# Kernel tuning notes

Measured on AMD Instinct MI355X. Metric: run time of the kernel, lower is better.

## Reference

```python
import jax, jax.numpy as jnp
import numpy as np
import math

B, S, H, D = 4, 1024, 12, 64   # batch, max_seqlen, heads, head_dim
DIM = H * D                    # 768
L = 512                        # actual per-sequence length (unpadded)
NNZ = B * L                    # total non-pad tokens


def setup_inputs() -> dict:
    key = jax.random.key(0)
    k1, k2, k3 = jax.random.split(key, 3)
    hidden_states = jax.random.normal(k1, (NNZ, DIM), dtype=jnp.float32)
    Wqkv_w = jax.random.normal(k2, (3 * DIM, DIM), dtype=jnp.float32) * 0.02
    Wqkv_b = jnp.zeros((3 * DIM,), dtype=jnp.float32)
    # attn mask: first L tokens of each sequence are real
    attn_mask = (jnp.arange(S)[None, :] < L).astype(jnp.int32) * jnp.ones((B, 1), jnp.int32)
    # additive bias (e.g. ALiBi/relative-pos style) + key-padding penalty
    bias = jax.random.normal(k3, (B, H, S, S), dtype=jnp.float32) * 0.02
    bias = bias + jnp.where(attn_mask[:, None, None, :] == 1, 0.0, -10000.0)
    # flattened positions of non-pad tokens in the padded (B*S,) layout
    indices = (jnp.arange(B)[:, None] * S + jnp.arange(L)[None, :]).reshape(-1).astype(jnp.int64)
    cu_seqlens = (jnp.arange(B + 1) * L).astype(jnp.int32)
    return {
        "hidden_states": hidden_states,
        "Wqkv_w": Wqkv_w,
        "Wqkv_b": Wqkv_b,
        "bias": bias,
        "cu_seqlens": cu_seqlens,
        "max_seqlen_in_batch": S,
        "indices": indices,
        "attn_mask": attn_mask,
    }


def reference(hidden_states, Wqkv_w, Wqkv_b, bias, cu_seqlens, max_seqlen_in_batch, indices, attn_mask):
    b = cu_seqlens.shape[0] - 1
    s = max_seqlen_in_batch
    # QKV projection on unpadded tokens: (nnz, 3*dim)
    qkv = hidden_states @ Wqkv_w.T + Wqkv_b
    # pad_input: scatter tokens into padded (b*s, 3*dim) buffer
    padded = jnp.zeros((b * s, 3 * DIM), dtype=qkv.dtype).at[indices].set(qkv)
    qkv = padded.reshape(b, s, 3, H, D)
    q = qkv[:, :, 0]  # (b, s, h, d)
    k = qkv[:, :, 1]
    v = qkv[:, :, 2]
    scores = jnp.einsum("bqhd,bkhd->bhqk", q, k) / math.sqrt(D) + bias
    probs = jax.nn.softmax(scores, axis=-1)  # dropout p=0 -> identity
    attn = jnp.einsum("bhqk,bkhd->bqhd", probs, v)  # (b, s, h, d)
    # unpad_input_only: gather non-pad rows, flatten heads
    out = attn.reshape(b * s, H * D)[indices]  # (nnz, dim)
    return out
```

## Files before the change

kernel.cpp:

```cpp
#include <hip/hip_runtime.h>
#include <hip/hip_bf16.h>


typedef __attribute__((ext_vector_type(8))) __bf16 bf16x8;
typedef __attribute__((ext_vector_type(4))) __bf16 bf16x4;
typedef __attribute__((ext_vector_type(4))) float  f32x4;

static __device__ __forceinline__ __bf16 tobf(float x) { return (__bf16)x; }

__global__ __launch_bounds__(256) void qkv_gemm(
    const float* __restrict__ hid,
    const float* __restrict__ W,
    const float* __restrict__ qb,
    __bf16* __restrict__ Qb, __bf16* __restrict__ Kb, __bf16* __restrict__ Vt)
{
    __shared__ char lds[2][24 * 1024];

    const int tid = threadIdx.x, lane = tid & 63, wave = tid >> 6;
    const int lo = lane & 15, hi = lane >> 4;
    const int wr = wave >> 1, wc = wave & 1;

    int flat = blockIdx.x;
    flat = (flat & 7) * 72 + (flat >> 3);
    const int f0 = (flat % 36) * 64;
    const int r0 = (flat / 36) * 128;

    const int srow = tid >> 3;
    const int kel  = (tid & 7) * 8;

    const float* abase = hid + (size_t)(r0 + srow) * 768 + kel;
    const float* bbase = W   + (size_t)(f0 + srow) * 768 + kel;

    float4 sa[6][2];
    auto LOADT = [&](int kt) {
        const int k0 = kt * 64;
#pragma unroll
        for (int p = 0; p < 4; ++p) {
            const float* a = abase + (size_t)p * 32 * 768 + k0;
            sa[p][0] = *reinterpret_cast<const float4*>(a);
            sa[p][1] = *reinterpret_cast<const float4*>(a + 4);
        }
#pragma unroll
        for (int p = 0; p < 2; ++p) {
            const float* bsrc = bbase + (size_t)p * 32 * 768 + k0;
            sa[4 + p][0] = *reinterpret_cast<const float4*>(bsrc);
            sa[4 + p][1] = *reinterpret_cast<const float4*>(bsrc + 4);
        }
    };
    auto STORET = [&](int buf) {
#pragma unroll
        for (int s = 0; s < 6; ++s) {
            const int row = (s < 4) ? s * 32 + srow : (s - 4) * 32 + srow;
            const int off = (s < 4) ? 0 : 16384;
            float4 x = sa[s][0], y = sa[s][1];
            bf16x8 o = { tobf(x.x), tobf(x.y), tobf(x.z), tobf(x.w),
                         tobf(y.x), tobf(y.y), tobf(y.z), tobf(y.w) };
            *reinterpret_cast<bf16x8*>(&lds[buf][off + row * 128 + ((kel * 2) ^ ((row & 7) << 4))]) = o;
        }
    };

    f32x4 acc[4][2] = {};
    LOADT(0); STORET(0);
    __syncthreads();

#pragma unroll 1
    for (int kt = 0; kt < 12; ++kt) {
        if (kt < 11) LOADT(kt + 1);
        const char* L = lds[kt & 1];
#pragma unroll
        for (int ks = 0; ks < 2; ++ks) {
            bf16x8 bfrag[2];
#pragma unroll
            for (int fn = 0; fn < 2; ++fn) {
                int row = wc * 32 + fn * 16 + lo;
                bfrag[fn] = *reinterpret_cast<const bf16x8*>(
                    L + 16384 + row * 128 + ((ks * 64 + hi * 16) ^ ((row & 7) << 4)));
            }
#pragma unroll
            for (int fm = 0; fm < 4; ++fm) {
                int row = wr * 64 + fm * 16 + lo;
                bf16x8 af = *reinterpret_cast<const bf16x8*>(
                    L + row * 128 + ((ks * 64 + hi * 16) ^ ((row & 7) << 4)));
                acc[fm][0] = __builtin_amdgcn_mfma_f32_16x16x32_bf16(af, bfrag[0], acc[fm][0], 0, 0, 0);
                acc[fm][1] = __builtin_amdgcn_mfma_f32_16x16x32_bf16(af, bfrag[1], acc[fm][1], 0, 0, 0);
            }
        }
        if (kt < 11) STORET((kt & 1) ^ 1);
        __syncthreads();
    }

#pragma unroll
    for (int fn = 0; fn < 2; ++fn) {
        int m = f0 + wc * 32 + fn * 16 + lo;
        float bv = qb[m];
        int sel = m / 768;
        int mm  = m - sel * 768;
        int hh  = mm >> 6, d = mm & 63;
        float scale = (sel == 0) ? 0.125f : 1.0f;
#pragma unroll
        for (int fm = 0; fm < 4; ++fm) {
            int t0 = r0 + wr * 64 + fm * 16 + hi * 4;
            int b  = t0 >> 9, q = t0 & 511;
            int bh = b * 12 + hh;
            float v[4];
#pragma unroll
            for (int j = 0; j < 4; ++j) v[j] = (acc[fm][fn][j] + bv) * scale;
            if (sel == 2) {
                bf16x4 pv = { tobf(v[0]), tobf(v[1]), tobf(v[2]), tobf(v[3]) };
                *reinterpret_cast<bf16x4*>(&Vt[((size_t)bh * 64 + d) * 512 + q]) = pv;
            } else {
                __bf16* dst = (sel == 0) ? Qb : Kb;
#pragma unroll
                for (int j = 0; j < 4; ++j)
                    dst[((size_t)bh * 512 + q + j) * 64 + d] = tobf(v[j]);
            }
        }
    }
}

__global__ __launch_bounds__(256) void attn_kernel(
    const __bf16* __restrict__ Qb, const __bf16* __restrict__ Kb,
    const __bf16* __restrict__ Vt, const float* __restrict__ bias,
    float* __restrict__ out)
{
    __shared__ __bf16 P[4][16][40];
    __shared__ float  Obuf[2][16][68];
    __shared__ float  Lbuf[2][16];

    const int tid = threadIdx.x, lane = tid & 63, wave = tid >> 6;
    const int lo = lane & 15, hi = lane >> 4;
    const int qt = wave >> 1, kp = wave & 1;

    int flat = blockIdx.x;
    flat = (flat & 7) * 96 + (flat >> 3);
    const int bh = flat >> 4, qtile = flat & 15;
    const int b = bh / 12, hd = bh % 12;
    const int q0 = qtile * 32 + qt * 16;

    const __bf16* Qp = Qb + ((size_t)bh * 512 + q0) * 64;
    bf16x8 qf0 = *reinterpret_cast<const bf16x8*>(Qp + lo * 64 + hi * 8);
    bf16x8 qf1 = *reinterpret_cast<const bf16x8*>(Qp + lo * 64 + 32 + hi * 8);

    const __bf16* Kbh = Kb + (size_t)bh * 512 * 64;
    const __bf16* Vbh = Vt + (size_t)bh * 64 * 512;
    const float*  bp  = bias + ((size_t)bh * 1024 + q0) * 1024;

    f32x4 c0[2], c1[2];
    bf16x8 kf[2][4], vf[2][4];
    auto LOADC = [&](int kc, int s) {
        const int k0 = kp * 256 + kc * 32;
#pragma unroll
        for (int j = 0; j < 4; ++j) {
            const float* r = bp + (size_t)(hi * 4 + j) * 1024 + k0;
            c0[s][j] = r[lo];
            c1[s][j] = r[16 + lo];
        }
        const __bf16* kr = Kbh + (size_t)(k0 + lo) * 64 + hi * 8;
        kf[s][0] = *reinterpret_cast<const bf16x8*>(kr);
        kf[s][1] = *reinterpret_cast<const bf16x8*>(kr + 32);
        kf[s][2] = *reinterpret_cast<const bf16x8*>(kr + 16 * 64);
        kf[s][3] = *reinterpret_cast<const bf16x8*>(kr + 16 * 64 + 32);
#pragma unroll
        for (int dt = 0; dt < 4; ++dt)
            vf[s][dt] = *reinterpret_cast<const bf16x8*>(
                Vbh + (size_t)(dt * 16 + lo) * 512 + k0 + hi * 8);
    };

    f32x4 oacc[4] = {};
    float lsum[4] = {0.f, 0.f, 0.f, 0.f};
    __bf16* Pw = &P[wave][0][0];

    LOADC(0, 0);
#pragma unroll
    for (int kc = 0; kc < 8; ++kc) {
        const int s = kc & 1;
        if (kc < 7) LOADC(kc + 1, s ^ 1);
        __builtin_amdgcn_s_setprio(1);
        f32x4 s0 = __builtin_amdgcn_mfma_f32_16x16x32_bf16(qf0, kf[s][0], c0[s], 0, 0, 0);
        s0       = __builtin_amdgcn_mfma_f32_16x16x32_bf16(qf1, kf[s][1], s0, 0, 0, 0);
        f32x4 s1 = __builtin_amdgcn_mfma_f32_16x16x32_bf16(qf0, kf[s][2], c1[s], 0, 0, 0);
        s1       = __builtin_amdgcn_mfma_f32_16x16x32_bf16(qf1, kf[s][3], s1, 0, 0, 0);
        __builtin_amdgcn_s_setprio(0);

#pragma unroll
        for (int j = 0; j < 4; ++j) {
            float p0 = __expf(s0[j]), p1 = __expf(s1[j]);
            lsum[j] += p0 + p1;
            Pw[(hi * 4 + j) * 40 + lo]      = tobf(p0);
            Pw[(hi * 4 + j) * 40 + 16 + lo] = tobf(p1);
        }
        bf16x8 pf = *reinterpret_cast<const bf16x8*>(Pw + lo * 40 + hi * 8);
        __builtin_amdgcn_s_setprio(1);
#pragma unroll
        for (int dt = 0; dt < 4; ++dt)
            oacc[dt] = __builtin_amdgcn_mfma_f32_16x16x32_bf16(pf, vf[s][dt], oacc[dt], 0, 0, 0);
        __builtin_amdgcn_s_setprio(0);
    }

#pragma unroll
    for (int j = 0; j < 4; ++j) {
        float s = lsum[j];
        s += __shfl_xor(s, 1, 64); s += __shfl_xor(s, 2, 64);
        s += __shfl_xor(s, 4, 64); s += __shfl_xor(s, 8, 64);
        lsum[j] = s;
    }

    if (kp == 1) {
#pragma unroll
        for (int dt = 0; dt < 4; ++dt)
#pragma unroll
            for (int j = 0; j < 4; ++j)
                Obuf[qt][hi * 4 + j][dt * 16 + lo] = oacc[dt][j];
        if (lo == 0) {
#pragma unroll
            for (int j = 0; j < 4; ++j) Lbuf[qt][hi * 4 + j] = lsum[j];
        }
    }
    __syncthreads();
    if (kp == 0) {
#pragma unroll
        for (int j = 0; j < 4; ++j) {
            float inv = 1.0f / (lsum[j] + Lbuf[qt][hi * 4 + j]);
            int q = q0 + hi * 4 + j;
            float* op = out + (size_t)(b * 512 + q) * 768 + hd * 64;
#pragma unroll
            for (int dt = 0; dt < 4; ++dt)
                op[dt * 16 + lo] = (oacc[dt][j] + Obuf[qt][hi * 4 + j][dt * 16 + lo]) * inv;
        }
    }
}

extern "C" void kernel_launch(void* const* d_in, const int* in_sizes, int n_in,
                              void* d_out, int out_size, void* d_ws, size_t ws_size,
                              hipStream_t stream) {
    const float* hid  = (const float*)d_in[0];
    const float* W    = (const float*)d_in[1];
    const float* qb   = (const float*)d_in[2];
    const float* bias = (const float*)d_in[3];
    float* out = (float*)d_out;

    char* ws = (char*)d_ws;
    __bf16* Qb = (__bf16*)(ws);
    __bf16* Kb = (__bf16*)(ws + 3145728);
    __bf16* Vt = (__bf16*)(ws + 6291456);

    qkv_gemm<<<576, 256, 0, stream>>>(hid, W, qb, Qb, Kb, Vt);
    attn_kernel<<<768, 256, 0, stream>>>(Qb, Kb, Vt, bias, out);
}
```

Baseline: 298.5 us.

## Pre-convert GEMM inputs to bf16, enlarge GEMM tile, deepen attention bias prefetch

Adds a separate kernel that converts hidden states and the QKV weight to bf16 in workspace, so the GEMM loads bf16 directly and skips per-tile conversion. The GEMM tile grows from 128x64 to 128x128, halving the grid and doubling per-wave accumulators. The attention kernel splits bias loads from K/V loads and prefetches the bias three chunks ahead in a triple buffer. This trades an extra launch and extra global traffic for the conversion pass against better latency hiding and operand reuse, at the cost of higher register pressure.

```diff
diff --git a/kernel.cpp b/kernel.cpp
--- a/kernel.cpp
+++ b/kernel.cpp
@@ -8,58 +8,66 @@
 
 static __device__ __forceinline__ __bf16 tobf(float x) { return (__bf16)x; }
 
+__global__ __launch_bounds__(256) void cvt_bf16(const float* __restrict__ hid,
+                                                const float* __restrict__ W,
+                                                __bf16* __restrict__ hidB,
+                                                __bf16* __restrict__ WB)
+{
+    int i = blockIdx.x * 256 + threadIdx.x;
+    const float* src; __bf16* dst; int off;
+    if (i < 196608) { src = hid; dst = hidB; off = i * 8; }
+    else            { src = W;   dst = WB;   off = (i - 196608) * 8; }
+    float4 a = *reinterpret_cast<const float4*>(src + off);
+    float4 b = *reinterpret_cast<const float4*>(src + off + 4);
+    bf16x8 o = { tobf(a.x), tobf(a.y), tobf(a.z), tobf(a.w),
+                 tobf(b.x), tobf(b.y), tobf(b.z), tobf(b.w) };
+    *reinterpret_cast<bf16x8*>(dst + off) = o;
+}
+
 __global__ __launch_bounds__(256) void qkv_gemm(
-    const float* __restrict__ hid,
-    const float* __restrict__ W,
-    const float* __restrict__ qb,
+    const __bf16* __restrict__ hidB,
+    const __bf16* __restrict__ WB,
+    const float*  __restrict__ qb,
     __bf16* __restrict__ Qb, __bf16* __restrict__ Kb, __bf16* __restrict__ Vt)
 {
-    __shared__ char lds[2][24 * 1024];
+    __shared__ char lds[2][32 * 1024];
 
     const int tid = threadIdx.x, lane = tid & 63, wave = tid >> 6;
     const int lo = lane & 15, hi = lane >> 4;
     const int wr = wave >> 1, wc = wave & 1;
 
     int flat = blockIdx.x;
-    flat = (flat & 7) * 72 + (flat >> 3);
-    const int f0 = (flat % 36) * 64;
-    const int r0 = (flat / 36) * 128;
+    flat = (flat & 7) * 36 + (flat >> 3);
+    const int f0 = (flat >> 4) * 128;
+    const int r0 = (flat & 15) * 128;
 
     const int srow = tid >> 3;
     const int kel  = (tid & 7) * 8;
 
-    const float* abase = hid + (size_t)(r0 + srow) * 768 + kel;
-    const float* bbase = W   + (size_t)(f0 + srow) * 768 + kel;
-
-    float4 sa[6][2];
+    const __bf16* abase = hidB + (size_t)(r0 + srow) * 768 + kel;
+    const __bf16* bbase = WB   + (size_t)(f0 + srow) * 768 + kel;
+
+    bf16x8 st[8];
     auto LOADT = [&](int kt) {
         const int k0 = kt * 64;
 #pragma unroll
-        for (int p = 0; p < 4; ++p) {
-            const float* a = abase + (size_t)p * 32 * 768 + k0;
-            sa[p][0] = *reinterpret_cast<const float4*>(a);
-            sa[p][1] = *reinterpret_cast<const float4*>(a + 4);
-        }
-#pragma unroll
-        for (int p = 0; p < 2; ++p) {
-            const float* bsrc = bbase + (size_t)p * 32 * 768 + k0;
-            sa[4 + p][0] = *reinterpret_cast<const float4*>(bsrc);
-            sa[4 + p][1] = *reinterpret_cast<const float4*>(bsrc + 4);
-        }
+        for (int p = 0; p < 4; ++p)
+            st[p]     = *reinterpret_cast<const bf16x8*>(abase + (size_t)p * 32 * 768 + k0);
+#pragma unroll
+        for (int p = 0; p < 4; ++p)
+            st[4 + p] = *reinterpret_cast<const bf16x8*>(bbase + (size_t)p * 32 * 768 + k0);
     };
     auto STORET = [&](int buf) {
 #pragma unroll
-        for (int s = 0; s < 6; ++s) {
-            const int row = (s < 4) ? s * 32 + srow : (s - 4) * 32 + srow;
+        for (int s = 0; s < 8; ++s) {
+            const int row = (s & 3) * 32 + srow;
             const int off = (s < 4) ? 0 : 16384;
-            float4 x = sa[s][0], y = sa[s][1];
-            bf16x8 o = { tobf(x.x), tobf(x.y), tobf(x.z), tobf(x.w),
-                         tobf(y.x), tobf(y.y), tobf(y.z), tobf(y.w) };
-            *reinterpret_cast<bf16x8*>(&lds[buf][off + row * 128 + ((kel * 2) ^ ((row & 7) << 4))]) = o;
-        }
-    };
-
-    f32x4 acc[4][2] = {};
+            *reinterpret_cast<bf16x8*>(
+                &lds[buf][off + row * 128 + ((kel * 2) ^ ((row & 7) << 4))]) = st[s];
+        }
+    };
+
+    f32x4 acc[4][4] = {};
     LOADT(0); STORET(0);
     __syncthreads();
 
@@ -69,10 +77,10 @@
         const char* L = lds[kt & 1];
 #pragma unroll
         for (int ks = 0; ks < 2; ++ks) {
-            bf16x8 bfrag[2];
-#pragma unroll
-            for (int fn = 0; fn < 2; ++fn) {
-                int row = wc * 32 + fn * 16 + lo;
+            bf16x8 bfrag[4];
+#pragma unroll
+            for (int fn = 0; fn < 4; ++fn) {
+                int row = wc * 64 + fn * 16 + lo;
                 bfrag[fn] = *reinterpret_cast<const bf16x8*>(
                     L + 16384 + row * 128 + ((ks * 64 + hi * 16) ^ ((row & 7) << 4)));
             }
@@ -81,8 +89,9 @@
                 int row = wr * 64 + fm * 16 + lo;
                 bf16x8 af = *reinterpret_cast<const bf16x8*>(
                     L + row * 128 + ((ks * 64 + hi * 16) ^ ((row & 7) << 4)));
-                acc[fm][0] = __builtin_amdgcn_mfma_f32_16x16x32_bf16(af, bfrag[0], acc[fm][0], 0, 0, 0);
-                acc[fm][1] = __builtin_amdgcn_mfma_f32_16x16x32_bf16(af, bfrag[1], acc[fm][1], 0, 0, 0);
+#pragma unroll
+                for (int fn = 0; fn < 4; ++fn)
+                    acc[fm][fn] = __builtin_amdgcn_mfma_f32_16x16x32_bf16(af, bfrag[fn], acc[fm][fn], 0, 0, 0);
             }
         }
         if (kt < 11) STORET((kt & 1) ^ 1);
@@ -90,8 +99,8 @@
     }
 
 #pragma unroll
-    for (int fn = 0; fn < 2; ++fn) {
-        int m = f0 + wc * 32 + fn * 16 + lo;
+    for (int fn = 0; fn < 4; ++fn) {
+        int m = f0 + wc * 64 + fn * 16 + lo;
         float bv = qb[m];
         int sel = m / 768;
         int mm  = m - sel * 768;
@@ -145,9 +154,9 @@
     const __bf16* Vbh = Vt + (size_t)bh * 64 * 512;
     const float*  bp  = bias + ((size_t)bh * 1024 + q0) * 1024;
 
-    f32x4 c0[2], c1[2];
+    f32x4 c0[3], c1[3];
     bf16x8 kf[2][4], vf[2][4];
-    auto LOADC = [&](int kc, int s) {
+    auto LOADB = [&](int kc, int s) {
         const int k0 = kp * 256 + kc * 32;
 #pragma unroll
         for (int j = 0; j < 4; ++j) {
@@ -155,6 +164,9 @@
             c0[s][j] = r[lo];
             c1[s][j] = r[16 + lo];
         }
+    };
+    auto LOADKV = [&](int kc, int s) {
+        const int k0 = kp * 256 + kc * 32;
         const __bf16* kr = Kbh + (size_t)(k0 + lo) * 64 + hi * 8;
         kf[s][0] = *reinterpret_cast<const bf16x8*>(kr);
         kf[s][1] = *reinterpret_cast<const bf16x8*>(kr + 32);
@@ -170,17 +182,19 @@
     float lsum[4] = {0.f, 0.f, 0.f, 0.f};
     __bf16* Pw = &P[wave][0][0];
 
-    LOADC(0, 0);
+    LOADB(0, 0); LOADB(1, 1); LOADB(2, 2);
+    LOADKV(0, 0);
 #pragma unroll
     for (int kc = 0; kc < 8; ++kc) {
-        const int s = kc & 1;
-        if (kc < 7) LOADC(kc + 1, s ^ 1);
+        const int sb = kc % 3, sk = kc & 1;
+        if (kc < 7) LOADKV(kc + 1, sk ^ 1);
         __builtin_amdgcn_s_setprio(1);
-        f32x4 s0 = __builtin_amdgcn_mfma_f32_16x16x32_bf16(qf0, kf[s][0], c0[s], 0, 0, 0);
-        s0       = __builtin_amdgcn_mfma_f32_16x16x32_bf16(qf1, kf[s][1], s0, 0, 0, 0);
-        f32x4 s1 = __builtin_amdgcn_mfma_f32_16x16x32_bf16(qf0, kf[s][2], c1[s], 0, 0, 0);
-        s1       = __builtin_amdgcn_mfma_f32_16x16x32_bf16(qf1, kf[s][3], s1, 0, 0, 0);
+        f32x4 s0 = __builtin_amdgcn_mfma_f32_16x16x32_bf16(qf0, kf[sk][0], c0[sb], 0, 0, 0);
+        s0       = __builtin_amdgcn_mfma_f32_16x16x32_bf16(qf1, kf[sk][1], s0, 0, 0, 0);
+        f32x4 s1 = __builtin_amdgcn_mfma_f32_16x16x32_bf16(qf0, kf[sk][2], c1[sb], 0, 0, 0);
+        s1       = __builtin_amdgcn_mfma_f32_16x16x32_bf16(qf1, kf[sk][3], s1, 0, 0, 0);
         __builtin_amdgcn_s_setprio(0);
+        if (kc < 5) LOADB(kc + 3, sb);
 
 #pragma unroll
         for (int j = 0; j < 4; ++j) {
@@ -193,7 +207,7 @@
         __builtin_amdgcn_s_setprio(1);
 #pragma unroll
         for (int dt = 0; dt < 4; ++dt)
-            oacc[dt] = __builtin_amdgcn_mfma_f32_16x16x32_bf16(pf, vf[s][dt], oacc[dt], 0, 0, 0);
+            oacc[dt] = __builtin_amdgcn_mfma_f32_16x16x32_bf16(pf, vf[sk][dt], oacc[dt], 0, 0, 0);
         __builtin_amdgcn_s_setprio(0);
     }
 
@@ -240,10 +254,13 @@
     float* out = (float*)d_out;
 
     char* ws = (char*)d_ws;
-    __bf16* Qb = (__bf16*)(ws);
-    __bf16* Kb = (__bf16*)(ws + 3145728);
-    __bf16* Vt = (__bf16*)(ws + 6291456);
-
-    qkv_gemm<<<576, 256, 0, stream>>>(hid, W, qb, Qb, Kb, Vt);
+    __bf16* hidB = (__bf16*)(ws);
+    __bf16* WB   = (__bf16*)(ws + 3145728);
+    __bf16* Qb   = (__bf16*)(ws + 6684672);
+    __bf16* Kb   = (__bf16*)(ws + 9830400);
+    __bf16* Vt   = (__bf16*)(ws + 12976128);
+
+    cvt_bf16<<<1632, 256, 0, stream>>>(hid, W, hidB, WB);
+    qkv_gemm<<<288, 256, 0, stream>>>(hidB, WB, qb, Qb, Kb, Vt);
     attn_kernel<<<768, 256, 0, stream>>>(Qb, Kb, Vt, bias, out);
 }
```

Measured after the change: 296.2 us. Within noise of the previous version (-0.8%).
